# Optimization experiments

Hardware: AMD Instinct MI355X
Metric: run time of the kernel (lower is better)

The kernel has to match this reference:

```python
import jax, jax.numpy as jnp
import numpy as np


def setup_inputs() -> dict:
    key = jax.random.key(0)
    k1, k2, k3, k4 = jax.random.split(key, 4)
    B, S, D = 8, 2048, 1024
    x = jax.random.normal(k1, (B, S, D), dtype=jnp.float32)
    scale = 1.0 / np.sqrt(D)  # glorot-ish magnitude
    Wq = jax.random.normal(k2, (D, D), dtype=jnp.float32) * scale
    Wk = jax.random.normal(k3, (D, D), dtype=jnp.float32) * scale
    Wv = jax.random.normal(k4, (D, D), dtype=jnp.float32) * scale
    return {"x": x, "Wq": Wq, "Wk": Wk, "Wv": Wv}


def reference(x, Wq, Wk, Wv):
    # q,k,v: [B,S,D]
    q = jnp.einsum("bsd,de->bse", x, Wq)
    k = jnp.einsum("bsd,de->bse", x, Wk)
    v = jnp.einsum("bsd,de->bse", x, Wv)
    d = k.shape[-1]
    # scores: [B,S,S], scaled by sqrt(d)
    scores = jnp.einsum("bqd,bkd->bqk", q, k) / jnp.sqrt(jnp.asarray(d, x.dtype))
    attn = jax.nn.softmax(scores, axis=-1)
    out = jnp.einsum("bqk,bkd->bqd", attn, v)
    return out
```

## Files before the change

### kernel.cpp

```cpp
#include <hip/hip_runtime.h>
#include <hip/hip_bf16.h>

typedef __bf16 bf16x8 __attribute__((ext_vector_type(8)));
typedef float  f32x4  __attribute__((ext_vector_type(4)));

static __device__ __forceinline__ unsigned short f2bf(float f) {
  unsigned int u = __float_as_uint(f);
  u += 0x7FFFu + ((u >> 16) & 1u);
  return (unsigned short)(u >> 16);
}

static __device__ __forceinline__ void gl_lds16(const void* g, void* l) {
  __builtin_amdgcn_global_load_lds(
      (const __attribute__((address_space(1))) void*)g,
      (__attribute__((address_space(3))) void*)l,
      16, 0, 0);
}

__global__ __launch_bounds__(256) void cast_f32_bf16(
    const float* __restrict__ in, unsigned short* __restrict__ out, int n) {
  int i = (blockIdx.x * 256 + threadIdx.x) * 4;
  const int stride = gridDim.x * 256 * 4;
  for (; i < n; i += stride) {
    float4 f = *(const float4*)(in + i);
    ushort4 o;
    o.x = f2bf(f.x); o.y = f2bf(f.y); o.z = f2bf(f.z); o.w = f2bf(f.w);
    *(ushort4*)(out + i) = o;
  }
}

__global__ __launch_bounds__(256) void transpose_cast_w(
    const float* __restrict__ w, unsigned short* __restrict__ wt) {
  __shared__ float tile[16][17];
  const int tx = threadIdx.x & 15, ty = threadIdx.x >> 4;
  const int bx = blockIdx.x * 16, by = blockIdx.y * 16;
  tile[ty][tx] = w[(size_t)(by + ty) * 1024 + bx + tx];
  __syncthreads();
  wt[(size_t)(bx + ty) * 1024 + by + tx] = f2bf(tile[tx][ty]);
}

template <int MODE>
__global__ __launch_bounds__(256, 2) void gemm_bt(
    const unsigned short* __restrict__ A, int lda, size_t astride,
    const unsigned short* __restrict__ B, int ldb, size_t bstride,
    int K, void* __restrict__ Cv, int ldc, size_t cstride,
    float* __restrict__ aux) {
  __shared__ __align__(16) unsigned char lds[16384];
  const unsigned d2 = blockIdx.x + gridDim.x * blockIdx.y;
  const unsigned ty = d2 % gridDim.y;
  const unsigned tx = d2 / gridDim.y;
  const int bn0 = tx * 128;
  const int bm0 = ty * 128;
  A += (size_t)blockIdx.z * astride;
  B += (size_t)blockIdx.z * bstride;

  const int tid = threadIdx.x;
  const int wid = tid >> 6, lane = tid & 63;
  const int wr = wid >> 1, wc = wid & 1;
  const int l15 = lane & 15, kq = lane >> 4;

  const int e0 = wid * 512 + lane * 8;
  const int r0 = e0 >> 5, c0 = e0 & 31;
  const size_t aoff0 = (size_t)(bm0 + r0) * lda + c0;
  const size_t aoff1 = (size_t)(bm0 + r0 + 64) * lda + c0;
  const size_t boff0 = (size_t)(bn0 + r0) * ldb + c0;
  const size_t boff1 = (size_t)(bn0 + r0 + 64) * ldb + c0;
  unsigned char* ldsA = lds + wid * 1024;
  unsigned char* ldsB = lds + 8192 + wid * 1024;

  f32x4 acc[4][4] = {};
  const int nkt = K >> 5;
  for (int kt = 0; kt < nkt; ++kt) {
    const int kc = kt << 5;
    gl_lds16(A + aoff0 + kc, ldsA);
    gl_lds16(A + aoff1 + kc, ldsA + 4096);
    gl_lds16(B + boff0 + kc, ldsB);
    gl_lds16(B + boff1 + kc, ldsB + 4096);
    __syncthreads();

    bf16x8 af[4], bg[4];
#pragma unroll
    for (int mi = 0; mi < 4; ++mi)
      af[mi] = *(const bf16x8*)(lds + ((wr * 64 + mi * 16 + l15) * 64 + kq * 16));
#pragma unroll
    for (int ni = 0; ni < 4; ++ni)
      bg[ni] = *(const bf16x8*)(lds + 8192 + ((wc * 64 + ni * 16 + l15) * 64 + kq * 16));
#pragma unroll
    for (int mi = 0; mi < 4; ++mi)
#pragma unroll
      for (int ni = 0; ni < 4; ++ni)
        acc[mi][ni] = __builtin_amdgcn_mfma_f32_16x16x32_bf16(af[mi], bg[ni], acc[mi][ni], 0, 0, 0);
    __syncthreads();
  }

  if constexpr (MODE == 3) {
#pragma unroll
    for (int mi = 0; mi < 4; ++mi)
#pragma unroll
      for (int ni = 0; ni < 4; ++ni)
#pragma unroll
        for (int r = 0; r < 4; ++r) {
          const int row = bm0 + wr * 64 + mi * 16 + kq * 4 + r;
          const int col = bn0 + wc * 64 + ni * 16 + l15;
          const float v = acc[mi][ni][r];
          unsigned short* q = (unsigned short*)Cv;
          if (col < 1024) {
            q[(size_t)row * 1024 + col] = f2bf(v);
          } else if (col < 2048) {
            q[16777216u + (size_t)row * 1024 + (col - 1024)] = f2bf(v);
          } else {
            const int b = row >> 11, s = row & 2047;
            q[33554432u + ((size_t)(b * 1024 + (col - 2048))) * 2048 + s] = f2bf(v);
          }
        }
  } else if constexpr (MODE == 4) {
    __shared__ float redsm[128][2];
    unsigned short* pp = (unsigned short*)Cv + (size_t)blockIdx.z * cstride;
    float rs[4][4];
#pragma unroll
    for (int mi = 0; mi < 4; ++mi)
#pragma unroll
      for (int r = 0; r < 4; ++r) rs[mi][r] = 0.f;
#pragma unroll
    for (int mi = 0; mi < 4; ++mi)
#pragma unroll
      for (int ni = 0; ni < 4; ++ni)
#pragma unroll
        for (int r = 0; r < 4; ++r) {
          const float e = exp2f(acc[mi][ni][r] * 0.045084220027780106f);
          rs[mi][r] += e;
          const int row = bm0 + wr * 64 + mi * 16 + kq * 4 + r;
          const int col = bn0 + wc * 64 + ni * 16 + l15;
          pp[(size_t)row * ldc + col] = f2bf(e);
        }
#pragma unroll
    for (int mi = 0; mi < 4; ++mi)
#pragma unroll
      for (int r = 0; r < 4; ++r) {
        float s = rs[mi][r];
        s += __shfl_xor(s, 1); s += __shfl_xor(s, 2);
        s += __shfl_xor(s, 4); s += __shfl_xor(s, 8);
        rs[mi][r] = s;
      }
    if (l15 == 0) {
#pragma unroll
      for (int mi = 0; mi < 4; ++mi)
#pragma unroll
        for (int r = 0; r < 4; ++r)
          redsm[wr * 64 + mi * 16 + kq * 4 + r][wc] = rs[mi][r];
    }
    __syncthreads();
    if (tid < 128)
      aux[((size_t)blockIdx.z * 16 + tx) * 2048 + bm0 + tid] =
          redsm[tid][0] + redsm[tid][1];
  } else {
    const float* inv = aux + (size_t)blockIdx.z * 2048;
    float* op = (float*)Cv + (size_t)blockIdx.z * cstride;
#pragma unroll
    for (int mi = 0; mi < 4; ++mi)
#pragma unroll
      for (int r = 0; r < 4; ++r) {
        const int row = bm0 + wr * 64 + mi * 16 + kq * 4 + r;
        const float iv = inv[row];
#pragma unroll
        for (int ni = 0; ni < 4; ++ni) {
          const int col = bn0 + wc * 64 + ni * 16 + l15;
          op[(size_t)row * ldc + col] = acc[mi][ni][r] * iv;
        }
      }
  }
}

__global__ __launch_bounds__(256) void combine_inv(
    const float* __restrict__ part, float* __restrict__ inv, int n) {
  const int i = blockIdx.x * 256 + threadIdx.x;
  if (i >= n) return;
  const int z = i >> 11, row = i & 2047;
  const float* p = part + ((size_t)z * 16) * 2048 + row;
  float s = 0.f;
#pragma unroll
  for (int j = 0; j < 16; ++j) s += p[j * 2048];
  inv[i] = 1.0f / s;
}

extern "C" void kernel_launch(void* const* d_in, const int* in_sizes, int n_in,
                              void* d_out, int out_size, void* d_ws, size_t ws_size,
                              hipStream_t stream) {
  const float* x  = (const float*)d_in[0];
  const float* Wq = (const float*)d_in[1];
  const float* Wk = (const float*)d_in[2];
  const float* Wv = (const float*)d_in[3];
  float* out = (float*)d_out;
  char* ws = (char*)d_ws;

  unsigned short* xb     = (unsigned short*)ws;
  unsigned short* wt_all = (unsigned short*)(ws + 33554432);
  unsigned short* qb     = (unsigned short*)(ws + 39845888);
  unsigned short* kb     = qb + 16777216;
  unsigned short* vt     = kb + 16777216;
  const size_t off_scores = 140509184ull;

  const size_t per_b = 8388608ull + 131072ull + 8192ull;
  int G; char *pPc, *partc, *invc;
  const size_t avail = ws_size > off_scores ? ws_size - off_scores : 0;
  G = (int)(avail / per_b); if (G > 8) G = 8;
  if (G >= 1) {
    pPc   = ws + off_scores;
    partc = pPc + (size_t)G * 8388608ull;
    invc  = partc + (size_t)G * 131072ull;
  } else {
    G = 2;
    pPc   = ws;
    partc = ws + 2 * 8388608ull;
    invc  = partc + 2 * 131072ull;
  }

  cast_f32_bf16<<<2048, 256, 0, stream>>>(x, xb, 16384 * 1024);
  transpose_cast_w<<<dim3(64, 64), 256, 0, stream>>>(Wq, wt_all);
  transpose_cast_w<<<dim3(64, 64), 256, 0, stream>>>(Wk, wt_all + 1048576);
  transpose_cast_w<<<dim3(64, 64), 256, 0, stream>>>(Wv, wt_all + 2097152);

  gemm_bt<3><<<dim3(24, 128), 256, 0, stream>>>(xb, 1024, 0, wt_all, 1024, 0,
                                                1024, qb, 0, 0, nullptr);

  for (int b0 = 0; b0 < 8; b0 += G) {
    const int g = (8 - b0) < G ? (8 - b0) : G;
    const size_t so = (size_t)b0 * 2097152;
    gemm_bt<4><<<dim3(16, 16, g), 256, 0, stream>>>(
        qb + so, 1024, 2097152, kb + so, 1024, 2097152, 1024,
        (unsigned short*)pPc, 2048, 4194304, (float*)partc);
    combine_inv<<<(g * 2048 + 255) / 256, 256, 0, stream>>>(
        (const float*)partc, (float*)invc, g * 2048);
    gemm_bt<5><<<dim3(8, 16, g), 256, 0, stream>>>(
        (const unsigned short*)pPc, 2048, 4194304,
        vt + so, 2048, 2097152, 2048,
        out + so, 1024, 2097152, (float*)invc);
  }
}
```

Before: 378.5 us.

## Triple-buffer LDS K-tiles with async prefetch and single barrier per step

Replaces the single-buffered load/sync/compute/sync GEMM loop with a three-stage LDS ring. Two K-tiles are prefetched ahead, and waits are handled with explicit vmcnt counts. LDS reads are issued as inline ds_read_b128, then the next stage's global-to-LDS load is issued before the MFMAs, with wave priority raised around the MFMA block. This aims to hide global memory latency behind compute and cut one barrier per iteration. The cost is LDS growing from 16KB to 48KB, which may reduce occupancy, and correctness now depends on hand-managed waitcnt counts.

Result: faster. 363.5 us (-4.0%).

```diff
diff --git a/kernel.cpp b/kernel.cpp
--- a/kernel.cpp
+++ b/kernel.cpp
@@ -45,7 +45,7 @@
     const unsigned short* __restrict__ B, int ldb, size_t bstride,
     int K, void* __restrict__ Cv, int ldc, size_t cstride,
     float* __restrict__ aux) {
-  __shared__ __align__(16) unsigned char lds[16384];
+  __shared__ __align__(16) unsigned char lds[49152];
   const unsigned d2 = blockIdx.x + gridDim.x * blockIdx.y;
   const unsigned ty = d2 % gridDim.y;
   const unsigned tx = d2 / gridDim.y;
@@ -65,33 +65,54 @@
   const size_t aoff1 = (size_t)(bm0 + r0 + 64) * lda + c0;
   const size_t boff0 = (size_t)(bn0 + r0) * ldb + c0;
   const size_t boff1 = (size_t)(bn0 + r0 + 64) * ldb + c0;
-  unsigned char* ldsA = lds + wid * 1024;
-  unsigned char* ldsB = lds + 8192 + wid * 1024;
+
+#define STAGE(t) do { \
+    unsigned char* s_ = lds + ((t) % 3) * 16384 + wid * 1024; \
+    const int kc_ = (t) << 5; \
+    gl_lds16(A + aoff0 + kc_, s_); \
+    gl_lds16(A + aoff1 + kc_, s_ + 4096); \
+    gl_lds16(B + boff0 + kc_, s_ + 8192); \
+    gl_lds16(B + boff1 + kc_, s_ + 12288); \
+  } while (0)
+#define DSR(dst, addr) asm volatile("ds_read_b128 %0, %1" : "=v"(dst) : "v"(addr))
+
+  const unsigned ldsbase =
+      (unsigned)(unsigned long long)(__attribute__((address_space(3))) unsigned char*)lds;
+  const unsigned aA = ldsbase + (wr * 64 + l15) * 64 + kq * 16;
+  const unsigned aB = ldsbase + 8192 + (wc * 64 + l15) * 64 + kq * 16;
 
   f32x4 acc[4][4] = {};
   const int nkt = K >> 5;
-  for (int kt = 0; kt < nkt; ++kt) {
-    const int kc = kt << 5;
-    gl_lds16(A + aoff0 + kc, ldsA);
-    gl_lds16(A + aoff1 + kc, ldsA + 4096);
-    gl_lds16(B + boff0 + kc, ldsB);
-    gl_lds16(B + boff1 + kc, ldsB + 4096);
-    __syncthreads();
-
+
+  STAGE(0);
+  STAGE(1);
+
+  for (int t = 0; t < nkt; ++t) {
+    if (t < nkt - 1) asm volatile("s_waitcnt vmcnt(4)" ::: "memory");
+    else             asm volatile("s_waitcnt vmcnt(0)" ::: "memory");
+    __builtin_amdgcn_s_barrier();
+
+    const unsigned so = (unsigned)(t % 3) * 16384u;
     bf16x8 af[4], bg[4];
 #pragma unroll
-    for (int mi = 0; mi < 4; ++mi)
-      af[mi] = *(const bf16x8*)(lds + ((wr * 64 + mi * 16 + l15) * 64 + kq * 16));
-#pragma unroll
-    for (int ni = 0; ni < 4; ++ni)
-      bg[ni] = *(const bf16x8*)(lds + 8192 + ((wc * 64 + ni * 16 + l15) * 64 + kq * 16));
+    for (int mi = 0; mi < 4; ++mi) DSR(af[mi], so + aA + mi * 1024);
+#pragma unroll
+    for (int ni = 0; ni < 4; ++ni) DSR(bg[ni], so + aB + ni * 1024);
+
+    if (t + 2 < nkt) STAGE(t + 2);
+
+    asm volatile("s_waitcnt lgkmcnt(0)" ::: "memory");
+    __builtin_amdgcn_sched_barrier(0);
+    __builtin_amdgcn_s_setprio(1);
 #pragma unroll
     for (int mi = 0; mi < 4; ++mi)
 #pragma unroll
       for (int ni = 0; ni < 4; ++ni)
         acc[mi][ni] = __builtin_amdgcn_mfma_f32_16x16x32_bf16(af[mi], bg[ni], acc[mi][ni], 0, 0, 0);
-    __syncthreads();
-  }
+    __builtin_amdgcn_s_setprio(0);
+  }
+#undef STAGE
+#undef DSR
 
   if constexpr (MODE == 3) {
 #pragma unroll
```
